# Kernel optimization log

Hardware: AMD Instinct MI355X
Metric: run time of the kernel (lower is better)

Reference implementation:

```python
import jax, jax.numpy as jnp
import numpy as np

Y, X, Z = 4096, 10000, 100
P_BU = 0.5                 # y_bottom_up_percent
P_TD = 1.0 - P_BU
SYN_AGE = 20.0
C_LO, C_HI = 0.8, 1.2      # synapse_coefficient


def _l2norm(w):
    # F.normalize(dim=1): divide by max(||row||, 1e-12)
    n = jnp.sqrt(jnp.sum(w * w, axis=1, keepdims=True))
    return w / jnp.maximum(n, 1e-12)


def setup_inputs() -> dict:
    key = jax.random.key(0)
    ks = jax.random.split(key, 9)
    return {
        "x": jax.random.normal(ks[0], (1, 100, 100), jnp.float32),
        "z": jax.random.randint(ks[1], (1,), 0, Z, jnp.int32),
        "w_x2y": jax.random.uniform(ks[2], (Y, X), jnp.float32),
        "w_z2y": jax.random.uniform(ks[3], (Y, Z), jnp.float32),
        "w_y2z": jax.random.uniform(ks[4], (Z, Y), jnp.float32),
        "x2y_diff": jax.random.uniform(ks[5], (Y, X), jnp.float32),
        "x2y_factor": jnp.ones((Y, X), jnp.float32),
        "y_age": jax.random.randint(ks[6], (Y,), 0, 40, jnp.int32),
        "y_thresh": jax.random.uniform(ks[7], (Y,), jnp.float32),
        "z_age": jax.random.randint(ks[8], (Z,), 0, 40, jnp.int32),
        "per_item": 1,
    }


def reference(x, z, w_x2y, w_z2y, w_y2z, x2y_diff, x2y_factor, y_age, y_thresh, z_age, per_item):
    # per_item loop in the original returns on the first iteration -> single step.
    x_n = _l2norm(x.reshape(1, -1))                      # [1, X]
    z_hot = jax.nn.one_hot(z, Z, dtype=jnp.float32)      # [1, Z] (already unit norm)
    c = z[0]

    # temporarily scaled + normalized weights used only for the response
    w_eff = _l2norm(w_x2y * x2y_factor)                  # [Y, X]
    w_z2y_n = _l2norm(w_z2y)                             # [Y, Z] (written back in torch)
    w_y2z_n = _l2norm(w_y2z)                             # [Z, Y] (written back in torch)

    y_bu = x_n @ w_eff.T                                 # [1, Y]
    y_td = z_hot @ w_z2y_n.T                             # [1, Y]
    pre = (P_BU * y_bu + P_TD * y_td)[0]                 # [Y]

    # top_k_competition(flag=1)
    y_age_f = y_age.astype(jnp.float32)
    idx0 = jnp.argmax(pre)
    max_resp = pre[idx0]
    keep = (max_resp > y_thresh[idx0]) | (y_age_f[idx0] < 1.0)
    unact = (y_age_f < 1.0).astype(pre.dtype)
    has_unact = jnp.sum(unact) > 0
    alt_idx = jnp.argmax(pre * unact)
    idx = jnp.where(keep | ~has_unact, idx0, alt_idx)

    # hebbian_learning: single-row indexed read-modify-write updates
    lr = 1.0 / (y_age_f[idx] + 1.0)
    new_w_row = (1.0 - lr) * w_x2y[idx] + lr * x_n[0]
    new_w_x2y = w_x2y.at[idx].set(new_w_row)

    new_diff_row = (1.0 - lr) * x2y_diff[idx] + lr * jnp.abs(new_w_row - x2y_diff[idx])
    new_diff = x2y_diff.at[idx].set(new_diff_row)

    # synapse maintenance over the full diff matrix
    mean_diff = jnp.mean(new_diff, axis=1, keepdims=True)   # [Y, 1]
    lower = C_LO * mean_diff
    upper = C_HI * mean_diff
    upper_flag = jnp.where(new_diff > upper, 0.0, 1.0)
    middle = (new_diff - upper) / jnp.maximum(lower - upper, 1e-12)
    nsf = jnp.where(new_diff < lower, 1.0, middle * upper_flag)
    new_factor = jnp.where(y_age_f[:, None] > SYN_AGE, nsf, x2y_factor)

    new_w_z2y = w_z2y_n.at[idx].set((1.0 - lr) * w_z2y_n[idx] + lr * z_hot[0])
    new_y_age = y_age_f.at[idx].add(1.0)

    z_age_f = z_age.astype(jnp.float32)
    lr_z = 1.0 / (z_age_f[c] + 1.0)
    y_resp = jnp.zeros((Y,), jnp.float32).at[idx].set(1.0)
    new_w_y2z = w_y2z_n.at[c].set((1.0 - lr_z) * w_y2z_n[c] + lr_z * y_resp)
    new_z_age = z_age_f.at[c].add(1.0)

    new_thresh = y_thresh.at[idx].set(lr * max_resp + (1.0 - lr) * y_thresh[idx])

    y_activated_num = jnp.sum(new_y_age >= 1.0).astype(jnp.int32)
    return (new_w_x2y, y_activated_num, new_w_z2y, new_w_y2z, new_diff,
            new_factor, new_y_age, new_z_age, new_thresh)
```

## Files before the change

### kernel.cpp

```cpp
#include <hip/hip_runtime.h>

constexpr int NX  = 10000;
constexpr int NX4 = NX / 4;
constexpr int NY  = 4096;
constexpr int NY4 = NY / 4;
constexpr int NZ  = 100;
constexpr int NT  = 256;
constexpr int KITER = (NX4 + NT - 1) / NT;

constexpr int WS_XSS  = 0;
constexpr int WS_DSUM = 1;
constexpr int WS_LR   = 2;
constexpr int WS_AGEI = 3;
constexpr int WS_IDX  = 4;
constexpr int WS_PRE  = 8;
constexpr int WS_ZNRM = 8 + NY;

using f4 = __attribute__((ext_vector_type(4))) float;

__device__ __forceinline__ double block_reduce(double v, double* sred) {
#pragma unroll
    for (int off = 32; off > 0; off >>= 1)
        v += __shfl_down(v, off, 64);
    int wid  = threadIdx.x >> 6;
    int lane = threadIdx.x & 63;
    __syncthreads();
    if (lane == 0) sred[wid] = v;
    __syncthreads();
    return sred[0] + sred[1] + sred[2] + sred[3];
}

__global__ __launch_bounds__(NT, 4) void k1(
    const float* __restrict__ x, const int* __restrict__ z,
    const float* __restrict__ w_x2y, const float* __restrict__ w_z2y,
    const float* __restrict__ diff, const float* __restrict__ factor,
    const int* __restrict__ y_age,
    float* __restrict__ out_w, float* __restrict__ out_wz,
    float* __restrict__ out_d, float* __restrict__ out_f,
    double* __restrict__ dws)
{
    __shared__ double sred[4];
    __shared__ double sbr[1];
    const int t = threadIdx.x;
    const int y = blockIdx.x;
    const size_t rb4 = (size_t)y * NX4;
    const f4* wr = (const f4*)w_x2y + rb4;
    const f4* fr = (const f4*)factor + rb4;
    const f4* dr = (const f4*)diff + rb4;
    const f4* xr = (const f4*)x;
    f4* o1 = (f4*)out_w + rb4;
    f4* o5 = (f4*)out_d + rb4;
    f4* o6 = (f4*)out_f + rb4;

    const int age = y_age[y];
    const bool young = ((double)age <= 20.0);

    const int c = z[0];
    float myz = 0.0f;
    if (t < NZ) myz = w_z2y[(size_t)y * NZ + t];

    f4 dv[KITER];
    double dot = 0.0, sq = 0.0, dsum = 0.0, xss = 0.0;
#pragma unroll
    for (int k = 0; k < KITER; ++k) {
        const int i = t + k * NT;
        if (i < NX4) {
            f4 wv = __builtin_nontemporal_load(wr + i);
            f4 fv = __builtin_nontemporal_load(fr + i);
            f4 d  = __builtin_nontemporal_load(dr + i);
            f4 xv = xr[i];
            dv[k] = d;
#pragma unroll
            for (int cc = 0; cc < 4; ++cc) {
                double wf = (double)wv[cc] * (double)fv[cc];
                dot  += (double)xv[cc] * wf;
                sq   += wf * wf;
                dsum += (double)d[cc];
                xss  += (double)xv[cc] * (double)xv[cc];
            }
            __builtin_nontemporal_store(wv, o1 + i);
            __builtin_nontemporal_store(d,  o5 + i);
            if (young) __builtin_nontemporal_store(fv, o6 + i);
        }
    }
    double dotT = block_reduce(dot,  sred);
    double sqT  = block_reduce(sq,   sred);
    double dsT  = block_reduce(dsum, sred);
    double xssT = block_reduce(xss,  sred);

    double zv = (t < NZ) ? (double)myz * (double)myz : 0.0;
    double zsq = block_reduce(zv, sred);
    double zn = sqrt(zsq); if (zn < 1e-12) zn = 1e-12;
    if (t < NZ) {
        out_wz[(size_t)y * NZ + t] = (float)((double)myz / zn);
        if (t == c) sbr[0] = (double)myz / zn;
    }
    __syncthreads();

    if (t == 0) {
        double xn = sqrt(xssT); if (xn < 1e-12) xn = 1e-12;
        double wn = sqrt(sqT);  if (wn < 1e-12) wn = 1e-12;
        double ybu = dotT / (xn * wn);
        dws[WS_PRE + y] = 0.5 * ybu + 0.5 * sbr[0];
        if (y == 0) { dws[WS_XSS] = xssT; dws[WS_DSUM] = 0.0; }
    }

    if (!young) {
        double mean  = dsT / (double)NX;
        double lower = 0.8 * mean, upper = 1.2 * mean;
        double den = lower - upper; if (den < 1e-12) den = 1e-12;
#pragma unroll
        for (int k = 0; k < KITER; ++k) {
            const int i = t + k * NT;
            if (i < NX4) {
                f4 d = dv[k];
                f4 nsf;
#pragma unroll
                for (int cc = 0; cc < 4; ++cc) {
                    double dd = (double)d[cc];
                    nsf[cc] = (float)((dd < lower) ? 1.0
                             : ((dd > upper) ? 0.0 : (dd - upper) / den));
                }
                __builtin_nontemporal_store(nsf, o6 + i);
            }
        }
    }
}

__global__ __launch_bounds__(NT) void k2(
    const float* __restrict__ w_y2z, float* __restrict__ out_yz, double* __restrict__ dws)
{
    __shared__ double sred[4];
    const int zr = blockIdx.x, t = threadIdx.x;
    const f4* r = (const f4*)w_y2z + (size_t)zr * NY4;
    f4* o = (f4*)out_yz + (size_t)zr * NY4;
    double sq = 0.0;
    for (int i = t; i < NY4; i += NT) {
        f4 v = r[i];
#pragma unroll
        for (int cc = 0; cc < 4; ++cc) sq += (double)v[cc] * (double)v[cc];
    }
    sq = block_reduce(sq, sred);
    double n = sqrt(sq); if (n < 1e-12) n = 1e-12;
    for (int i = t; i < NY4; i += NT) {
        f4 v = r[i]; f4 ov;
#pragma unroll
        for (int cc = 0; cc < 4; ++cc) ov[cc] = (float)((double)v[cc] / n);
        o[i] = ov;
    }
    if (t == 0) dws[WS_ZNRM + zr] = n;
}

__global__ __launch_bounds__(NT) void k3(
    const int* __restrict__ z, const float* __restrict__ w_z2y,
    const float* __restrict__ w_y2z, const int* __restrict__ y_age,
    const float* __restrict__ y_thresh, const int* __restrict__ z_age,
    float* __restrict__ out_act, float* __restrict__ out_wz,
    float* __restrict__ out_yz, float* __restrict__ out_yage,
    float* __restrict__ out_zage, float* __restrict__ out_th,
    double* __restrict__ dws)
{
    __shared__ double sval[NT];
    __shared__ int    sidx[NT];
    __shared__ int    scnt[NT];
    __shared__ double sh[8];
    __shared__ double sred[4];
    const int t = threadIdx.x;
    const int c = z[0];

    double bv = -1e300; int bi = 0;
    for (int yy = t; yy < NY; yy += NT) {
        double v = dws[WS_PRE + yy];
        if (v > bv) { bv = v; bi = yy; }
    }
    sval[t] = bv; sidx[t] = bi;
    __syncthreads();
    for (int s = NT / 2; s > 0; s >>= 1) {
        if (t < s) {
            double ov = sval[t + s]; int oi = sidx[t + s];
            if (ov > sval[t] || (ov == sval[t] && oi < sidx[t])) { sval[t] = ov; sidx[t] = oi; }
        }
        __syncthreads();
    }
    if (t == 0) { sh[0] = sval[0]; sh[1] = (double)sidx[0]; }
    __syncthreads();
    const int idx0 = (int)sh[1];
    const double max_resp = sh[0];

    double bv2 = -1e300; int bi2 = 0; int un_cnt = 0;
    for (int yy = t; yy < NY; yy += NT) {
        int un = (y_age[yy] < 1) ? 1 : 0;
        un_cnt += un;
        double v = dws[WS_PRE + yy] * (double)un;
        if (v > bv2) { bv2 = v; bi2 = yy; }
    }
    sval[t] = bv2; sidx[t] = bi2; scnt[t] = un_cnt;
    __syncthreads();
    for (int s = NT / 2; s > 0; s >>= 1) {
        if (t < s) {
            double ov = sval[t + s]; int oi = sidx[t + s];
            if (ov > sval[t] || (ov == sval[t] && oi < sidx[t])) { sval[t] = ov; sidx[t] = oi; }
            scnt[t] += scnt[t + s];
        }
        __syncthreads();
    }
    if (t == 0) {
        int alt = sidx[0];
        bool has_un = (scnt[0] > 0);
        bool keep = (max_resp > (double)y_thresh[idx0]) || (y_age[idx0] < 1);
        int idx = (keep || !has_un) ? idx0 : alt;
        double agei = (double)y_age[idx];
        double lr = 1.0 / (agei + 1.0);
        double lrz = 1.0 / ((double)z_age[c] + 1.0);
        dws[WS_LR] = lr; dws[WS_AGEI] = agei; dws[WS_IDX] = (double)idx;
        sh[2] = (double)idx; sh[3] = lr; sh[4] = lrz; sh[5] = lr * max_resp;
    }
    __syncthreads();
    const int idx = (int)sh[2];
    const double lr = sh[3], lrz = sh[4];

    int actcnt = 0;
    for (int yy = t; yy < NY; yy += NT) {
        int age = y_age[yy];
        int na = age + ((yy == idx) ? 1 : 0);
        out_yage[yy] = (float)na;
        actcnt += (na >= 1) ? 1 : 0;
        float th = y_thresh[yy];
        out_th[yy] = (yy == idx) ? (float)(sh[5] + (1.0 - lr) * (double)th) : th;
    }
    scnt[t] = actcnt;
    __syncthreads();
    for (int s = NT / 2; s > 0; s >>= 1) {
        if (t < s) scnt[t] += scnt[t + s];
        __syncthreads();
    }
    if (t == 0) out_act[0] = (float)scnt[0];

    if (t < NZ) out_zage[t] = (float)(z_age[t] + ((t == c) ? 1 : 0));

    double zv = 0.0; float myz = 0.0f;
    if (t < NZ) { myz = w_z2y[(size_t)idx * NZ + t]; zv = (double)myz * (double)myz; }
    double zsq = block_reduce(zv, sred);
    double zn = sqrt(zsq); if (zn < 1e-12) zn = 1e-12;
    if (t < NZ) {
        double wn = (double)myz / zn;
        out_wz[(size_t)idx * NZ + t] =
            (float)((1.0 - lr) * wn + lr * ((t == c) ? 1.0 : 0.0));
    }

    double nc = dws[WS_ZNRM + c];
    const f4* wy = (const f4*)w_y2z + (size_t)c * NY4;
    f4* oy = (f4*)out_yz + (size_t)c * NY4;
    for (int i = t; i < NY4; i += NT) {
        f4 wv = wy[i]; f4 ov;
#pragma unroll
        for (int cc = 0; cc < 4; ++cc) {
            int yy = 4 * i + cc;
            double w = (double)wv[cc] / nc;
            ov[cc] = (float)((1.0 - lrz) * w + lrz * ((yy == idx) ? 1.0 : 0.0));
        }
        oy[i] = ov;
    }
}

__global__ __launch_bounds__(NT) void k4(
    const float* __restrict__ x, const float* __restrict__ w_x2y,
    const float* __restrict__ diff,
    float* __restrict__ out_w, float* __restrict__ out_d,
    double* __restrict__ dws)
{
    __shared__ double sred[4];
    const int idx = (int)dws[WS_IDX];
    const double lr = dws[WS_LR];
    double nx = sqrt(dws[WS_XSS]); if (nx < 1e-12) nx = 1e-12;
    const int i = blockIdx.x * NT + threadIdx.x;
    const size_t rb4 = (size_t)idx * NX4;
    double nds = 0.0;
    if (i < NX4) {
        f4 wv = ((const f4*)w_x2y + rb4)[i];
        f4 dv = ((const f4*)diff + rb4)[i];
        f4 xv = ((const f4*)x)[i];
        f4 ow, od;
#pragma unroll
        for (int cc = 0; cc < 4; ++cc) {
            double nw = (1.0 - lr) * (double)wv[cc] + lr * ((double)xv[cc] / nx);
            double d0 = (double)dv[cc];
            double nd = (1.0 - lr) * d0 + lr * fabs(nw - d0);
            ow[cc] = (float)nw;
            od[cc] = (float)nd;
            nds += nd;
        }
        ((f4*)out_w + rb4)[i] = ow;
        ((f4*)out_d + rb4)[i] = od;
    }
    double s = block_reduce(nds, sred);
    if (threadIdx.x == 0) atomicAdd(&dws[WS_DSUM], s);
}

__global__ __launch_bounds__(NT) void k5(
    const float* __restrict__ x, const float* __restrict__ w_x2y,
    const float* __restrict__ diff, float* __restrict__ out_f,
    double* __restrict__ dws)
{
    if (dws[WS_AGEI] <= 20.0) return;
    const int idx = (int)dws[WS_IDX];
    const double lr = dws[WS_LR];
    double nx = sqrt(dws[WS_XSS]); if (nx < 1e-12) nx = 1e-12;
    double mean = dws[WS_DSUM] / (double)NX;
    double lower = 0.8 * mean, upper = 1.2 * mean;
    double den = lower - upper; if (den < 1e-12) den = 1e-12;
    const int i = blockIdx.x * NT + threadIdx.x;
    if (i >= NX4) return;
    const size_t rb4 = (size_t)idx * NX4;
    f4 wv = ((const f4*)w_x2y + rb4)[i];
    f4 dv = ((const f4*)diff + rb4)[i];
    f4 xv = ((const f4*)x)[i];
    f4 of;
#pragma unroll
    for (int cc = 0; cc < 4; ++cc) {
        double nw = (1.0 - lr) * (double)wv[cc] + lr * ((double)xv[cc] / nx);
        double d0 = (double)dv[cc];
        double nd = (1.0 - lr) * d0 + lr * fabs(nw - d0);
        of[cc] = (float)((nd < lower) ? 1.0 : ((nd > upper) ? 0.0 : (nd - upper) / den));
    }
    ((f4*)out_f + rb4)[i] = of;
}

extern "C" void kernel_launch(void* const* d_in, const int* in_sizes, int n_in,
                              void* d_out, int out_size, void* d_ws, size_t ws_size,
                              hipStream_t stream) {
    const float* x        = (const float*)d_in[0];
    const int*   z        = (const int*)  d_in[1];
    const float* w_x2y    = (const float*)d_in[2];
    const float* w_z2y    = (const float*)d_in[3];
    const float* w_y2z    = (const float*)d_in[4];
    const float* diff     = (const float*)d_in[5];
    const float* factor   = (const float*)d_in[6];
    const int*   y_age    = (const int*)  d_in[7];
    const float* y_thresh = (const float*)d_in[8];
    const int*   z_age    = (const int*)  d_in[9];

    float* out = (float*)d_out;
    float* o1 = out;
    float* o2 = o1 + (size_t)NY * NX;
    float* o3 = o2 + 1;
    float* o4 = o3 + (size_t)NY * NZ;
    float* o5 = o4 + (size_t)NZ * NY;
    float* o6 = o5 + (size_t)NY * NX;
    float* o7 = o6 + (size_t)NY * NX;
    float* o8 = o7 + NY;
    float* o9 = o8 + NZ;

    double* dws = (double*)d_ws;

    k1<<<NY, NT, 0, stream>>>(x, z, w_x2y, w_z2y, diff, factor, y_age,
                              o1, o3, o5, o6, dws);
    k2<<<NZ, NT, 0, stream>>>(w_y2z, o4, dws);
    k3<<<1, NT, 0, stream>>>(z, w_z2y, w_y2z, y_age, y_thresh, z_age,
                             o2, o3, o4, o7, o8, o9, dws);
    k4<<<(NX4 + NT - 1) / NT, NT, 0, stream>>>(x, w_x2y, diff, o1, o5, dws);
    k5<<<(NX4 + NT - 1) / NT, NT, 0, stream>>>(x, w_x2y, diff, o6, dws);
}
```

Before: 855.2 us.

## Software-pipeline row loads in k1 and stage diff row in LDS

Replaces the fully unrolled register array of diff values with a 4-deep rotating prefetch of weight, factor, diff and x vectors, so loads for later iterations are issued while earlier ones are consumed. The diff row is kept in a 40 KB shared-memory buffer for the later synapse-factor pass instead of in registers. The diff-sum accumulation and its reduction are skipped for young rows, where they are not used. This lowers register pressure, but the large LDS allocation limits how many blocks fit per CU and may reduce occupancy.

```diff
diff --git a/kernel.cpp b/kernel.cpp
--- a/kernel.cpp
+++ b/kernel.cpp
@@ -7,6 +7,7 @@
 constexpr int NZ  = 100;
 constexpr int NT  = 256;
 constexpr int KITER = (NX4 + NT - 1) / NT;
+constexpr int PD = 4;
 
 constexpr int WS_XSS  = 0;
 constexpr int WS_DSUM = 1;
@@ -39,6 +40,7 @@
     float* __restrict__ out_d, float* __restrict__ out_f,
     double* __restrict__ dws)
 {
+    __shared__ f4     sdiff[NX4];
     __shared__ double sred[4];
     __shared__ double sbr[1];
     const int t = threadIdx.x;
@@ -59,24 +61,50 @@
     float myz = 0.0f;
     if (t < NZ) myz = w_z2y[(size_t)y * NZ + t];
 
-    f4 dv[KITER];
+    f4 ws_[PD], fs_[PD], ds_[PD], xs_[PD];
+#pragma unroll
+    for (int k = 0; k < PD - 1; ++k) {
+        const int i = t + k * NT;
+        ws_[k] = __builtin_nontemporal_load(wr + i);
+        fs_[k] = __builtin_nontemporal_load(fr + i);
+        ds_[k] = __builtin_nontemporal_load(dr + i);
+        xs_[k] = xr[i];
+    }
+
     double dot = 0.0, sq = 0.0, dsum = 0.0, xss = 0.0;
 #pragma unroll
     for (int k = 0; k < KITER; ++k) {
+        const int kp = k + PD - 1;
+        if (kp < KITER) {
+            const int ip = t + kp * NT;
+            const int sp = kp % PD;
+            if (kp < KITER - 1) {
+                ws_[sp] = __builtin_nontemporal_load(wr + ip);
+                fs_[sp] = __builtin_nontemporal_load(fr + ip);
+                ds_[sp] = __builtin_nontemporal_load(dr + ip);
+                xs_[sp] = xr[ip];
+            } else if (ip < NX4) {
+                ws_[sp] = __builtin_nontemporal_load(wr + ip);
+                fs_[sp] = __builtin_nontemporal_load(fr + ip);
+                ds_[sp] = __builtin_nontemporal_load(dr + ip);
+                xs_[sp] = xr[ip];
+            }
+        }
         const int i = t + k * NT;
-        if (i < NX4) {
-            f4 wv = __builtin_nontemporal_load(wr + i);
-            f4 fv = __builtin_nontemporal_load(fr + i);
-            f4 d  = __builtin_nontemporal_load(dr + i);
-            f4 xv = xr[i];
-            dv[k] = d;
+        if (k < KITER - 1 || i < NX4) {
+            const int s = k % PD;
+            f4 wv = ws_[s], fv = fs_[s], d = ds_[s], xv = xs_[s];
+            sdiff[i] = d;
 #pragma unroll
             for (int cc = 0; cc < 4; ++cc) {
                 double wf = (double)wv[cc] * (double)fv[cc];
                 dot  += (double)xv[cc] * wf;
                 sq   += wf * wf;
-                dsum += (double)d[cc];
                 xss  += (double)xv[cc] * (double)xv[cc];
+            }
+            if (!young) {
+#pragma unroll
+                for (int cc = 0; cc < 4; ++cc) dsum += (double)d[cc];
             }
             __builtin_nontemporal_store(wv, o1 + i);
             __builtin_nontemporal_store(d,  o5 + i);
@@ -85,8 +113,8 @@
     }
     double dotT = block_reduce(dot,  sred);
     double sqT  = block_reduce(sq,   sred);
-    double dsT  = block_reduce(dsum, sred);
     double xssT = block_reduce(xss,  sred);
+    double dsT  = young ? 0.0 : block_reduce(dsum, sred);
 
     double zv = (t < NZ) ? (double)myz * (double)myz : 0.0;
     double zsq = block_reduce(zv, sred);
@@ -112,8 +140,8 @@
 #pragma unroll
         for (int k = 0; k < KITER; ++k) {
             const int i = t + k * NT;
-            if (i < NX4) {
-                f4 d = dv[k];
+            if (k < KITER - 1 || i < NX4) {
+                f4 d = sdiff[i];
                 f4 nsf;
 #pragma unroll
                 for (int cc = 0; cc < 4; ++cc) {
```

Result: no change. 871.1 us (+1.9%).
